# Optimization experiments

Hardware: AMD Instinct MI355X
Metric: run time of the kernel (lower is better)

Reference implementation:

```python
import jax, jax.numpy as jnp
import numpy as np

EPS = 1e-9
ALPHA = 1.0
BETA = 6.0
TOPK = 13
NUM_CLASSES = 80


def _make_boxes(key, shape, img=640.0, wh_min=8.0, wh_max=128.0):
    k1, k2 = jax.random.split(key)
    cxy = jax.random.uniform(k1, shape[:-1] + (2,)) * img
    wh = wh_min + jax.random.uniform(k2, shape[:-1] + (2,)) * (wh_max - wh_min)
    return jnp.concatenate([cxy - wh / 2, cxy + wh / 2], axis=-1)


def setup_inputs() -> dict:
    key = jax.random.key(0)
    ks = jax.random.split(key, 5)
    B, N, C, M = 16, 8400, NUM_CLASSES, 64
    pd_scores = jax.random.normal(ks[0], (B, N, C), dtype=jnp.float32)  # logits
    pd_bboxes = _make_boxes(ks[1], (B, N, 4))
    anc_points = jax.random.uniform(ks[2], (N, 2)) * 640.0
    gt_labels = jax.random.randint(ks[3], (B, M, 1), 0, C).astype(jnp.int64)
    gt_bboxes = _make_boxes(ks[4], (B, M, 4), wh_min=16.0, wh_max=256.0)
    mask_gt = jnp.ones((B, M, 1), dtype=jnp.float32)
    return {"pd_scores": pd_scores, "pd_bboxes": pd_bboxes, "anc_points": anc_points,
            "gt_labels": gt_labels, "gt_bboxes": gt_bboxes, "mask_gt": mask_gt}


def _pairwise_iou(gt_bboxes, pd_bboxes):
    # gt: (B,M,4), pd: (B,N,4) -> (B,M,N)
    a1 = gt_bboxes[:, :, None, :2]
    a2 = gt_bboxes[:, :, None, 2:]
    b1 = pd_bboxes[:, None, :, :2]
    b2 = pd_bboxes[:, None, :, 2:]
    inter = jnp.clip(jnp.minimum(a2, b2) - jnp.maximum(a1, b1), 0.0).prod(-1)
    area_a = (a2 - a1).prod(-1)
    area_b = (b2 - b1).prod(-1)
    return inter / jnp.maximum(area_a + area_b - inter, EPS)


def _tal_assign(pd_scores, pd_bboxes, anc_points, gt_labels, gt_bboxes, mask_gt):
    B, N, C = pd_scores.shape
    M = gt_labels.shape[1]
    ps = jax.nn.sigmoid(pd_scores)  # input_is_logits=True
    mask_gt_bool = mask_gt[..., 0] > 0.5  # (B,M)

    # centers-in-boxes mask (B,M,N)
    xy = anc_points[None, None, :, :]
    lt = gt_bboxes[:, :, None, :2]
    rb = gt_bboxes[:, :, None, 2:]
    deltas = jnp.concatenate([xy - lt, rb - xy], axis=-1)  # (B,M,N,4)
    mask_in_gts = deltas.min(-1) > EPS
    valid = mask_in_gts & mask_gt_bool[:, :, None]

    # alignment metric: score(gt class)^alpha * IoU^beta, zero outside valid
    gt_ids = jnp.clip(gt_labels[..., 0], 0)  # (B,M)
    scores_t = jnp.swapaxes(ps, 1, 2)  # (B,C,N)
    bbox_scores = jnp.take_along_axis(scores_t, gt_ids[:, :, None], axis=1)  # (B,M,N)
    ious = _pairwise_iou(gt_bboxes, pd_bboxes)
    ious = jnp.where(valid, ious, 0.0)
    align = jnp.where(valid, (bbox_scores ** ALPHA) * (ious ** BETA), 0.0)

    # top-k anchors per GT along anchor dim
    topv, topi = jax.lax.top_k(align, TOPK)  # (B,M,K)
    sel = (topv > EPS) & mask_gt_bool[:, :, None]
    bi = jnp.arange(B)[:, None, None]
    mi = jnp.arange(M)[None, :, None]
    cnt = jnp.zeros((B, M, N), jnp.int32).at[bi, mi, topi].add(sel.astype(jnp.int32))
    topk_mask = cnt > 0
    mask_pos = (topk_mask & valid).astype(jnp.float32)  # (B,M,N)

    # resolve anchors assigned to multiple GTs: keep highest IoU GT
    fg = mask_pos.sum(axis=1)  # (B,N)
    multi = (fg > 1)[:, None, :]  # (B,1,N)
    best_gt = jnp.argmax(ious, axis=1)  # (B,N)
    is_max = jnp.swapaxes(jax.nn.one_hot(best_gt, M, dtype=mask_pos.dtype), 1, 2)  # (B,M,N)
    mask_pos = jnp.where(multi, is_max, mask_pos)
    fg_mask = mask_pos.sum(axis=1)  # (B,N)
    tgt_gt_idx = jnp.argmax(mask_pos, axis=1)  # (B,N)

    # gather targets
    target_labels = jnp.take_along_axis(gt_labels[..., 0], tgt_gt_idx, axis=1)  # (B,N)
    target_bboxes = jnp.take_along_axis(gt_bboxes, tgt_gt_idx[..., None], axis=1)  # (B,N,4)

    # normalized classification targets
    align = align * mask_pos
    max_align = align.max(axis=1, keepdims=True) + EPS  # (B,1,N)
    per_anchor = (align / max_align * (ious * mask_pos)).sum(axis=1)  # (B,N)
    onehot = jax.nn.one_hot(target_labels, C, dtype=jnp.float32)
    cls_targets = onehot * per_anchor[..., None]  # (B,N,C)
    return target_labels, target_bboxes, cls_targets, fg_mask > 0, tgt_gt_idx


def reference(pd_scores, pd_bboxes, anc_points, gt_labels, gt_bboxes, mask_gt):
    return _tal_assign(pd_scores, pd_bboxes, anc_points, gt_labels, gt_bboxes, mask_gt)
```

## Files before the change

kernel.cpp:

```cpp
#include <hip/hip_runtime.h>
#include <math.h>

#define BB 16
#define NN 8400
#define CC 80
#define MM 64
#define KTOP 13
#define FEPS 1e-9f
#define CAP 2048
#define RPW 8

typedef float floatx4 __attribute__((ext_vector_type(4)));
typedef unsigned long long u64;

#define OFF_O1 134400
#define OFF_O2 672000
#define OFF_O3 11424000
#define OFF_O4 11558400

#define ZERO_N (1024 + 3 * 134400)

__device__ __forceinline__ float iou_pair(const float4 g, const float4 p) {
    float ix1 = fmaxf(g.x, p.x);
    float iy1 = fmaxf(g.y, p.y);
    float ix2 = fminf(g.z, p.z);
    float iy2 = fminf(g.w, p.w);
    float iw = fmaxf(ix2 - ix1, 0.0f);
    float ih = fmaxf(iy2 - iy1, 0.0f);
    float inter = iw * ih;
    float aa = (g.z - g.x) * (g.w - g.y);
    float ab = (p.z - p.x) * (p.w - p.y);
    float uni = fmaxf(aa + ab - inter, FEPS);
    return inter / uni;
}

__global__ __launch_bounds__(256) void k_zero(int* __restrict__ p)
{
    int i = blockIdx.x * 256 + threadIdx.x;
    if (i < ZERO_N) p[i] = 0;
}

__global__ __launch_bounds__(256) void k_align_emit(
    const float* __restrict__ pd_scores, const float* __restrict__ pd_bboxes,
    const float* __restrict__ anc, const int* __restrict__ gt_labels,
    const float* __restrict__ gt_bboxes, const float* __restrict__ mask_gt,
    int* __restrict__ ccnt, u64* __restrict__ cand)
{
    const int b = blockIdx.y;
    const int n0 = blockIdx.x * 64;
    const int tid = threadIdx.x;
    const int a = tid >> 2;
    const int q = tid & 3;

    __shared__ float4 srows4[1280];
    __shared__ float4 gtb[MM];
    __shared__ float4 pbbS[64];
    __shared__ float2 ancS[64];
    __shared__ int    labS[MM];
    __shared__ unsigned short maskS16[256];
    __shared__ int hcnt[MM], hslot[MM], gbase[MM];

    const float4* src4 = (const float4*)(pd_scores + (size_t)b * NN * CC);
    const int base4 = n0 * 20;
    const int lim = NN * 20 - base4;
    float4 r0 = (tid        < lim) ? src4[base4 + tid       ] : make_float4(0,0,0,0);
    float4 r1 = (tid + 256  < lim) ? src4[base4 + tid + 256 ] : make_float4(0,0,0,0);
    float4 r2 = (tid + 512  < lim) ? src4[base4 + tid + 512 ] : make_float4(0,0,0,0);
    float4 r3 = (tid + 768  < lim) ? src4[base4 + tid + 768 ] : make_float4(0,0,0,0);
    float4 r4 = (tid + 1024 < lim) ? src4[base4 + tid + 1024] : make_float4(0,0,0,0);

    if (tid < MM) {
        float4 g = *(const float4*)&gt_bboxes[(size_t)(b * MM + tid) * 4];
        if (mask_gt[b * MM + tid] <= 0.5f)
            g = make_float4(1e30f, 1e30f, -1e30f, -1e30f);
        gtb[tid] = g;
        int lb = gt_labels[b * MM + tid];
        labS[tid] = lb > 0 ? lb : 0;
        hcnt[tid] = 0;
        hslot[tid] = 0;
    }
    if (tid < 64) {
        int gn = n0 + tid;
        pbbS[tid] = (gn < NN)
            ? *(const float4*)&pd_bboxes[((size_t)b * NN + gn) * 4]
            : make_float4(0.f, 0.f, 0.f, 0.f);
        ancS[tid] = (gn < NN) ? *(const float2*)&anc[2 * gn]
                              : make_float2(0.f, 0.f);
    }
    __syncthreads();

    {
        unsigned short pm = 0;
        if (n0 + a < NN) {
            float ax = ancS[a].x, ay = ancS[a].y;
            #pragma unroll
            for (int mm = 0; mm < 16; ++mm) {
                float4 g = gtb[q * 16 + mm];
                float d1 = ax - g.x, d2 = ay - g.y;
                float d3 = g.z - ax, d4 = g.w - ay;
                if (fminf(fminf(d1, d2), fminf(d3, d4)) > FEPS)
                    pm |= (unsigned short)(1u << mm);
            }
        }
        maskS16[tid] = pm;
        unsigned t16 = pm;
        while (t16) {
            int mm = __ffs(t16) - 1; t16 &= t16 - 1;
            atomicAdd(&hcnt[q * 16 + mm], 1);
        }
    }
    srows4[tid       ] = r0;
    srows4[tid + 256 ] = r1;
    srows4[tid + 512 ] = r2;
    srows4[tid + 768 ] = r3;
    srows4[tid + 1024] = r4;
    __syncthreads();

    if (tid < MM && hcnt[tid] > 0)
        gbase[tid] = atomicAdd(&ccnt[b * MM + tid], hcnt[tid]);
    __syncthreads();

    {
        unsigned t16 = maskS16[tid];
        if (t16) {
            const float4 p = pbbS[a];
            const float* row = (const float*)srows4 + a * 80;
            const int gn = n0 + a;
            while (t16) {
                int mm = __ffs(t16) - 1; t16 &= t16 - 1;
                int m = q * 16 + mm;
                float io = iou_pair(gtb[m], p);
                float x = row[labS[m]];
                float s = 1.0f / (1.0f + expf(-x));
                float i2 = io * io;
                unsigned key = __float_as_uint(s * (i2 * i2 * i2));
                int slot = gbase[m] + atomicAdd(&hslot[m], 1);
                if (slot < CAP)
                    cand[(size_t)(b * MM + m) * CAP + slot] =
                        ((u64)key << 32) | (unsigned)(NN - gn);
            }
        }
    }
}

__global__ __launch_bounds__(256) void k_topk(
    const int* __restrict__ ccnt, const u64* __restrict__ cand,
    int* __restrict__ cntb, int* __restrict__ mselb, float* __restrict__ aselb)
{
    const int bm = blockIdx.x;
    const int b = bm >> 6, m = bm & 63;
    const int tid = threadIdx.x;
    const int lane = tid & 63;
    const int wid = tid >> 6;

    __shared__ u64 cmerge[64];

    const unsigned epskey = __float_as_uint(FEPS);
    const int count = min(ccnt[bm], CAP);
    const u64* list = cand + (size_t)bm * CAP;

    u64 e[RPW];
    #pragma unroll
    for (int j = 0; j < RPW; ++j) {
        int i = tid + j * 256;
        e[j] = (i < count) ? list[i] : 0ull;
    }

    {
        u64 lm = 0ull;
        #pragma unroll
        for (int j = 0; j < RPW; ++j) if (e[j] > lm) lm = e[j];

        u64 winv = 0ull;
        for (int r = 0; r < KTOP; ++r) {
            u64 bv = lm;
            #pragma unroll
            for (int off = 32; off > 0; off >>= 1) {
                u64 ov = __shfl_xor(bv, off, 64);
                if (ov > bv) bv = ov;
            }
            if ((unsigned)(bv >> 32) <= epskey) break;
            if (lane == r) winv = bv;
            if (lm == bv) {
                #pragma unroll
                for (int j = 0; j < RPW; ++j) if (e[j] == bv) e[j] = 0ull;
                lm = 0ull;
                #pragma unroll
                for (int j = 0; j < RPW; ++j) if (e[j] > lm) lm = e[j];
            }
        }
        if (lane < KTOP) cmerge[wid * KTOP + lane] = winv;
        if (wid == 0 && lane >= 4 * KTOP) cmerge[lane] = 0ull;
    }
    __syncthreads();

    if (wid == 0) {
        u64 v = cmerge[lane];
        u64 winv = 0ull;
        for (int r = 0; r < KTOP; ++r) {
            u64 bv = v;
            #pragma unroll
            for (int off = 32; off > 0; off >>= 1) {
                u64 ov = __shfl_xor(bv, off, 64);
                if (ov > bv) bv = ov;
            }
            if ((unsigned)(bv >> 32) <= epskey) break;
            if (lane == r) winv = bv;
            if (v == bv) v = 0ull;
        }
        if (lane < KTOP) {
            unsigned hk = (unsigned)(winv >> 32);
            if (hk > epskey) {
                int n = NN - (int)(winv & 0xFFFFFFFFull);
                int ai = b * NN + n;
                atomicAdd(&cntb[ai], 1);
                atomicAdd(&mselb[ai], m);
                atomicAdd(&aselb[ai], __uint_as_float(hk));
            }
        }
    }
}

__global__ __launch_bounds__(256) void k_assign_cls(
    const float* __restrict__ pd_scores, const float* __restrict__ pd_bboxes,
    const float* __restrict__ anc, const int* __restrict__ gt_labels,
    const float* __restrict__ gt_bboxes, const float* __restrict__ mask_gt,
    const int* __restrict__ cntb, const int* __restrict__ mselb,
    const float* __restrict__ aselb,
    float* __restrict__ out0, float* __restrict__ out1,
    float* __restrict__ out3, float* __restrict__ out4,
    floatx4* __restrict__ cls4)
{
    const int b = blockIdx.y;
    const int n0 = blockIdx.x * 256;
    const int tid = threadIdx.x;
    const int n = n0 + tid;

    __shared__ float4 gtb[MM];
    __shared__ int    labS[MM];
    __shared__ float  mgS[MM];
    __shared__ int    labL[256];
    __shared__ float  perL[256];

    if (tid < MM) {
        int m = tid;
        gtb[m]  = *(const float4*)&gt_bboxes[(size_t)(b * MM + m) * 4];
        labS[m] = gt_labels[b * MM + m];
        mgS[m]  = mask_gt[b * MM + m];
    }
    __syncthreads();

    float per = 0.0f, fg = 0.0f;
    int mstar = 0;

    if (n < NN) {
        const size_t idx = (size_t)b * NN + n;
        const int cnt = cntb[idx];
        if (cnt > 0) {
            fg = 1.0f;
            const float4 p = *(const float4*)&pd_bboxes[idx * 4];
            if (cnt == 1) {
                mstar = mselb[idx];
                float a = aselb[idx];
                float io = iou_pair(gtb[mstar], p);
                per = a / (a + FEPS) * io;
            } else {
                float2 a2 = *(const float2*)&anc[2 * n];
                float bestI = -1.0f; int bestM = 0;
                for (int m = 0; m < MM; ++m) {
                    float4 gg = gtb[m];
                    float d1 = a2.x - gg.x, d2 = a2.y - gg.y;
                    float d3 = gg.z - a2.x, d4 = gg.w - a2.y;
                    bool valid = (fminf(fminf(d1, d2), fminf(d3, d4)) > FEPS) &&
                                 (mgS[m] > 0.5f);
                    float io = valid ? iou_pair(gg, p) : 0.0f;
                    if (io > bestI) { bestI = io; bestM = m; }
                }
                mstar = bestM;
                float io = bestI;
                int lb = labS[mstar]; int lbc = lb > 0 ? lb : 0;
                float x = pd_scores[idx * CC + lbc];
                float s = 1.0f / (1.0f + expf(-x));
                float i2 = io * io;
                float a = s * (i2 * i2 * i2);
                per = a / (a + FEPS) * io;
            }
        }
        out0[idx] = (float)labS[mstar];
        ((float4*)out1)[idx] = gtb[mstar];
        out3[idx] = fg;
        out4[idx] = (float)mstar;
    }
    labL[tid] = (n < NN) ? labS[mstar] : 0;
    perL[tid] = per;
    __syncthreads();

    const size_t base4 = ((size_t)b * NN + n0) * 20;
    for (int k = tid; k < 5120; k += 256) {
        int lrow = k / 20;
        int gn = n0 + lrow;
        if (gn >= NN) break;
        int c4 = (k - lrow * 20) * 4;
        int lab = labL[lrow];
        float pr = perL[lrow];
        int d = lab - c4;
        floatx4 v;
        v.x = (d == 0) ? pr : 0.0f;
        v.y = (d == 1) ? pr : 0.0f;
        v.z = (d == 2) ? pr : 0.0f;
        v.w = (d == 3) ? pr : 0.0f;
        __builtin_nontemporal_store(v, &cls4[base4 + k]);
    }
}

extern "C" void kernel_launch(void* const* d_in, const int* in_sizes, int n_in,
                              void* d_out, int out_size, void* d_ws, size_t ws_size,
                              hipStream_t stream) {
    const float* pd_scores = (const float*)d_in[0];
    const float* pd_bboxes = (const float*)d_in[1];
    const float* anc       = (const float*)d_in[2];
    const int*   gt_labels = (const int*)d_in[3];
    const float* gt_bboxes = (const float*)d_in[4];
    const float* mask_gt   = (const float*)d_in[5];

    float* out  = (float*)d_out;
    float* out0 = out;
    float* out1 = out + OFF_O1;
    float* out2 = out + OFF_O2;
    float* out3 = out + OFF_O3;
    float* out4 = out + OFF_O4;

    int*   ws_i  = (int*)d_ws;
    int*   ccnt  = ws_i;
    int*   cntb  = ws_i + 1024;
    int*   mselb = ws_i + 1024 + 134400;
    float* aselb = (float*)(ws_i + 1024 + 2 * 134400);
    u64*   cand  = (u64*)((char*)d_ws + (size_t)ZERO_N * 4);

    k_zero<<<dim3((ZERO_N + 255) / 256), dim3(256), 0, stream>>>(ws_i);

    k_align_emit<<<dim3((NN + 63) / 64, BB), dim3(256), 0, stream>>>(
        pd_scores, pd_bboxes, anc, gt_labels, gt_bboxes, mask_gt, ccnt, cand);

    k_topk<<<dim3(BB * MM), dim3(256), 0, stream>>>(
        ccnt, cand, cntb, mselb, aselb);

    k_assign_cls<<<dim3((NN + 255) / 256, BB), dim3(256), 0, stream>>>(
        pd_scores, pd_bboxes, anc, gt_labels, gt_bboxes, mask_gt,
        cntb, mselb, aselb, out0, out1, out3, out4, (floatx4*)out2);
}
```

Before: 61.79 us.

## Emit default outputs in align kernel and resolve only positive anchors sparsely

Background outputs (zeroed class targets, label and box of GT 0, fg=0) are now written by the align kernel, which already touches every anchor. Top-k winners are appended to a per-batch compact list instead of dense per-anchor atomic arrays. A new 16-block resolve kernel fixes up only the positive anchors, counting duplicates in shared memory. The zero kernel is replaced by a small memset, removing the dense assign pass and its large workspace. The risk is that the resolve kernel runs on only 16 blocks, its list is capped at 1024 entries, and it assumes its writes land after the background writes from the earlier kernel.

```diff
diff --git a/kernel.cpp b/kernel.cpp
--- a/kernel.cpp
+++ b/kernel.cpp
@@ -18,7 +18,9 @@
 #define OFF_O3 11424000
 #define OFF_O4 11558400
 
-#define ZERO_N (1024 + 3 * 134400)
+#define POSL_OFF 4160
+#define CAND_OFF 135232
+#define ZERO_BYTES 4160
 
 __device__ __forceinline__ float iou_pair(const float4 g, const float4 p) {
     float ix1 = fmaxf(g.x, p.x);
@@ -34,17 +36,14 @@
     return inter / uni;
 }
 
-__global__ __launch_bounds__(256) void k_zero(int* __restrict__ p)
-{
-    int i = blockIdx.x * 256 + threadIdx.x;
-    if (i < ZERO_N) p[i] = 0;
-}
-
 __global__ __launch_bounds__(256) void k_align_emit(
     const float* __restrict__ pd_scores, const float* __restrict__ pd_bboxes,
     const float* __restrict__ anc, const int* __restrict__ gt_labels,
     const float* __restrict__ gt_bboxes, const float* __restrict__ mask_gt,
-    int* __restrict__ ccnt, u64* __restrict__ cand)
+    int* __restrict__ ccnt, u64* __restrict__ cand,
+    float* __restrict__ out0, float* __restrict__ out1,
+    float* __restrict__ out3, float* __restrict__ out4,
+    floatx4* __restrict__ cls4)
 {
     const int b = blockIdx.y;
     const int n0 = blockIdx.x * 64;
@@ -141,11 +140,32 @@
             }
         }
     }
+
+    {
+        const float lab0 = (float)gt_labels[b * MM];
+        const float4 g0 = *(const float4*)&gt_bboxes[(size_t)b * MM * 4];
+        const floatx4 z = {0.f, 0.f, 0.f, 0.f};
+        const size_t cbase4 = ((size_t)b * NN + n0) * 20;
+        for (int k = tid; k < 1280; k += 256) {
+            int gn = n0 + k / 20;
+            if (gn < NN) __builtin_nontemporal_store(z, &cls4[cbase4 + k]);
+        }
+        if (tid < 64) {
+            int gn = n0 + tid;
+            if (gn < NN) {
+                size_t idx = (size_t)b * NN + gn;
+                out0[idx] = lab0;
+                ((float4*)out1)[idx] = g0;
+                out3[idx] = 0.0f;
+                out4[idx] = 0.0f;
+            }
+        }
+    }
 }
 
 __global__ __launch_bounds__(256) void k_topk(
     const int* __restrict__ ccnt, const u64* __restrict__ cand,
-    int* __restrict__ cntb, int* __restrict__ mselb, float* __restrict__ aselb)
+    int* __restrict__ poscnt, u64* __restrict__ poslist)
 {
     const int bm = blockIdx.x;
     const int b = bm >> 6, m = bm & 63;
@@ -212,104 +232,94 @@
             unsigned hk = (unsigned)(winv >> 32);
             if (hk > epskey) {
                 int n = NN - (int)(winv & 0xFFFFFFFFull);
-                int ai = b * NN + n;
-                atomicAdd(&cntb[ai], 1);
-                atomicAdd(&mselb[ai], m);
-                atomicAdd(&aselb[ai], __uint_as_float(hk));
-            }
-        }
-    }
-}
-
-__global__ __launch_bounds__(256) void k_assign_cls(
+                int pos = atomicAdd(&poscnt[b], 1);
+                if (pos < 1024)
+                    poslist[(size_t)b * 1024 + pos] =
+                        ((u64)hk << 20) | ((u64)n << 6) | (u64)m;
+            }
+        }
+    }
+}
+
+__global__ __launch_bounds__(256) void k_resolve(
+    const int* __restrict__ poscnt, const u64* __restrict__ poslist,
     const float* __restrict__ pd_scores, const float* __restrict__ pd_bboxes,
     const float* __restrict__ anc, const int* __restrict__ gt_labels,
     const float* __restrict__ gt_bboxes, const float* __restrict__ mask_gt,
-    const int* __restrict__ cntb, const int* __restrict__ mselb,
-    const float* __restrict__ aselb,
     float* __restrict__ out0, float* __restrict__ out1,
     float* __restrict__ out3, float* __restrict__ out4,
-    floatx4* __restrict__ cls4)
+    float* __restrict__ cls)
 {
-    const int b = blockIdx.y;
-    const int n0 = blockIdx.x * 256;
+    const int b = blockIdx.x;
     const int tid = threadIdx.x;
-    const int n = n0 + tid;
-
-    __shared__ float4 gtb[MM];
-    __shared__ int    labS[MM];
-    __shared__ float  mgS[MM];
-    __shared__ int    labL[256];
-    __shared__ float  perL[256];
-
+
+    __shared__ unsigned cntL[NN];
+    __shared__ float4 gtbR[MM];
+    __shared__ int    labR[MM];
+    __shared__ float  mgR[MM];
+
+    for (int i = tid; i < NN; i += 256) cntL[i] = 0u;
     if (tid < MM) {
-        int m = tid;
-        gtb[m]  = *(const float4*)&gt_bboxes[(size_t)(b * MM + m) * 4];
-        labS[m] = gt_labels[b * MM + m];
-        mgS[m]  = mask_gt[b * MM + m];
-    }
-    __syncthreads();
-
-    float per = 0.0f, fg = 0.0f;
-    int mstar = 0;
-
-    if (n < NN) {
+        gtbR[tid] = *(const float4*)&gt_bboxes[(size_t)(b * MM + tid) * 4];
+        labR[tid] = gt_labels[b * MM + tid];
+        mgR[tid]  = mask_gt[b * MM + tid];
+    }
+    __syncthreads();
+
+    const int np = min(poscnt[b], 1024);
+    const u64* list = poslist + (size_t)b * 1024;
+
+    for (int i = tid; i < np; i += 256) {
+        int n = (int)((list[i] >> 6) & 0x3FFF);
+        atomicAdd(&cntL[n], 1u);
+    }
+    __syncthreads();
+
+    for (int i = tid; i < np; i += 256) {
+        const u64 e = list[i];
+        const unsigned hk = (unsigned)(e >> 20);
+        const int n = (int)((e >> 6) & 0x3FFF);
+        const int m = (int)(e & 63);
         const size_t idx = (size_t)b * NN + n;
-        const int cnt = cntb[idx];
-        if (cnt > 0) {
-            fg = 1.0f;
-            const float4 p = *(const float4*)&pd_bboxes[idx * 4];
-            if (cnt == 1) {
-                mstar = mselb[idx];
-                float a = aselb[idx];
-                float io = iou_pair(gtb[mstar], p);
-                per = a / (a + FEPS) * io;
-            } else {
-                float2 a2 = *(const float2*)&anc[2 * n];
-                float bestI = -1.0f; int bestM = 0;
-                for (int m = 0; m < MM; ++m) {
-                    float4 gg = gtb[m];
-                    float d1 = a2.x - gg.x, d2 = a2.y - gg.y;
-                    float d3 = gg.z - a2.x, d4 = gg.w - a2.y;
-                    bool valid = (fminf(fminf(d1, d2), fminf(d3, d4)) > FEPS) &&
-                                 (mgS[m] > 0.5f);
-                    float io = valid ? iou_pair(gg, p) : 0.0f;
-                    if (io > bestI) { bestI = io; bestM = m; }
-                }
-                mstar = bestM;
-                float io = bestI;
-                int lb = labS[mstar]; int lbc = lb > 0 ? lb : 0;
-                float x = pd_scores[idx * CC + lbc];
-                float s = 1.0f / (1.0f + expf(-x));
-                float i2 = io * io;
-                float a = s * (i2 * i2 * i2);
-                per = a / (a + FEPS) * io;
-            }
-        }
-        out0[idx] = (float)labS[mstar];
-        ((float4*)out1)[idx] = gtb[mstar];
-        out3[idx] = fg;
+        const unsigned c = cntL[n] & 0xFFFFu;
+
+        int mstar; float per;
+        const float4 p = *(const float4*)&pd_bboxes[idx * 4];
+        if (c == 1) {
+            mstar = m;
+            float a = __uint_as_float(hk);
+            float io = iou_pair(gtbR[mstar], p);
+            per = a / (a + FEPS) * io;
+        } else {
+            unsigned old = atomicOr(&cntL[n], 0x80000000u);
+            if (old & 0x80000000u) continue;
+            float2 a2 = *(const float2*)&anc[2 * n];
+            float bestI = -1.0f; int bestM = 0;
+            for (int m2 = 0; m2 < MM; ++m2) {
+                float4 gg = gtbR[m2];
+                float d1 = a2.x - gg.x, d2 = a2.y - gg.y;
+                float d3 = gg.z - a2.x, d4 = gg.w - a2.y;
+                bool valid = (fminf(fminf(d1, d2), fminf(d3, d4)) > FEPS) &&
+                             (mgR[m2] > 0.5f);
+                float io = valid ? iou_pair(gg, p) : 0.0f;
+                if (io > bestI) { bestI = io; bestM = m2; }
+            }
+            mstar = bestM;
+            float io = bestI;
+            int lb = labR[mstar]; int lbc = lb > 0 ? lb : 0;
+            float x = pd_scores[idx * CC + lbc];
+            float s = 1.0f / (1.0f + expf(-x));
+            float i2 = io * io;
+            float a = s * (i2 * i2 * i2);
+            per = a / (a + FEPS) * io;
+        }
+
+        out0[idx] = (float)labR[mstar];
+        ((float4*)out1)[idx] = gtbR[mstar];
+        out3[idx] = 1.0f;
         out4[idx] = (float)mstar;
-    }
-    labL[tid] = (n < NN) ? labS[mstar] : 0;
-    perL[tid] = per;
-    __syncthreads();
-
-    const size_t base4 = ((size_t)b * NN + n0) * 20;
-    for (int k = tid; k < 5120; k += 256) {
-        int lrow = k / 20;
-        int gn = n0 + lrow;
-        if (gn >= NN) break;
-        int c4 = (k - lrow * 20) * 4;
-        int lab = labL[lrow];
-        float pr = perL[lrow];
-        int d = lab - c4;
-        floatx4 v;
-        v.x = (d == 0) ? pr : 0.0f;
-        v.y = (d == 1) ? pr : 0.0f;
-        v.z = (d == 2) ? pr : 0.0f;
-        v.w = (d == 3) ? pr : 0.0f;
-        __builtin_nontemporal_store(v, &cls4[base4 + k]);
+        int lab = labR[mstar];
+        if (lab >= 0 && lab < CC) cls[idx * CC + lab] = per;
     }
 }
 
@@ -330,22 +340,21 @@
     float* out3 = out + OFF_O3;
     float* out4 = out + OFF_O4;
 
-    int*   ws_i  = (int*)d_ws;
-    int*   ccnt  = ws_i;
-    int*   cntb  = ws_i + 1024;
-    int*   mselb = ws_i + 1024 + 134400;
-    float* aselb = (float*)(ws_i + 1024 + 2 * 134400);
-    u64*   cand  = (u64*)((char*)d_ws + (size_t)ZERO_N * 4);
-
-    k_zero<<<dim3((ZERO_N + 255) / 256), dim3(256), 0, stream>>>(ws_i);
+    int*   ccnt    = (int*)d_ws;
+    int*   poscnt  = (int*)d_ws + 1024;
+    u64*   poslist = (u64*)((char*)d_ws + POSL_OFF);
+    u64*   cand    = (u64*)((char*)d_ws + CAND_OFF);
+
+    hipMemsetAsync(d_ws, 0, ZERO_BYTES, stream);
 
     k_align_emit<<<dim3((NN + 63) / 64, BB), dim3(256), 0, stream>>>(
-        pd_scores, pd_bboxes, anc, gt_labels, gt_bboxes, mask_gt, ccnt, cand);
+        pd_scores, pd_bboxes, anc, gt_labels, gt_bboxes, mask_gt,
+        ccnt, cand, out0, out1, out3, out4, (floatx4*)out2);
 
     k_topk<<<dim3(BB * MM), dim3(256), 0, stream>>>(
-        ccnt, cand, cntb, mselb, aselb);
-
-    k_assign_cls<<<dim3((NN + 255) / 256, BB), dim3(256), 0, stream>>>(
-        pd_scores, pd_bboxes, anc, gt_labels, gt_bboxes, mask_gt,
-        cntb, mselb, aselb, out0, out1, out3, out4, (floatx4*)out2);
-}
+        ccnt, cand, poscnt, poslist);
+
+    k_resolve<<<dim3(BB), dim3(256), 0, stream>>>(
+        poscnt, poslist, pd_scores, pd_bboxes, anc, gt_labels, gt_bboxes,
+        mask_gt, out0, out1, out3, out4, out2);
+}
```

Measured after the change: 82.52 us. 1.34x slower.
